# Kernel tuning notes

Measured on AMD Instinct MI355X. Metric: run time of the kernel, lower is better.

The kernel has to match this reference:

```python
import jax, jax.numpy as jnp
import numpy as np

B, C, KF, VF, H, W = 16, 128, 128, 128, 128, 128


def setup_inputs() -> dict:
    key = jax.random.key(0)
    k1, k2, k3, k4, k5 = jax.random.split(key, 5)
    x = jax.random.normal(k1, (B, C, H, W), dtype=jnp.float32)
    # 1x1 conv weights (flattened to [out_ch, in_ch]); small init so raw exp stays finite
    qk_w = jax.random.normal(k2, (2 * KF, 2 * C), dtype=jnp.float32) * 0.02
    qk_b = jnp.zeros((2 * KF,), dtype=jnp.float32)
    v_w = jax.random.normal(k3, (VF, C), dtype=jnp.float32) * 0.02
    v_b = jnp.zeros((VF,), dtype=jnp.float32)
    return {"x": x, "qk_w": qk_w, "qk_b": qk_b, "v_w": v_w, "v_b": v_b}


def reference(x, qk_w, qk_b, v_w, v_b):
    Bc, Cc, Hc, Wc = x.shape
    # qk 1x1 conv on channel-doubled input: (B, 2*KF, H, W)
    x_qk = jnp.concatenate([x, x], axis=1)
    qk = jnp.einsum('oc,bchw->bohw', qk_w, x_qk) + qk_b[None, :, None, None]
    q, k = jnp.split(qk, 2, axis=1)  # each (B, KF, H, W)
    # scores over row positions: contract the W axis -> (B, KF, H, H)
    scores = jnp.einsum('bfhw,bfgw->bfhg', q, k) * (Cc ** -0.5)
    # hand-rolled causal softmax: raw exp * lower-triangular mask / sum (no max subtraction, faithful)
    mask = jnp.tril(jnp.ones((Hc, Hc), dtype=scores.dtype))  # mask[r, c] = 1 iff r >= c
    masked_exps = jnp.exp(scores) * mask[None, None, :, :]
    causal_softmax = masked_exps / masked_exps.sum(axis=-1, keepdims=True)
    # v 1x1 conv: (B, VF, H, W)
    v = jnp.einsum('oc,bchw->bohw', v_w, x) + v_b[None, :, None, None]
    # einsum 'jilm,jklm->jklm' == v * sum over the KF axis of the softmax
    out = v * causal_softmax.sum(axis=1, keepdims=True)
    return out
```

## Files before the change

kernel.cpp:

```cpp
#include <hip/hip_runtime.h>
#include <hip/hip_bf16.h>


using short8 = __attribute__((ext_vector_type(8))) short;
using f32x4  = __attribute__((ext_vector_type(4))) float;
typedef unsigned short u16;
typedef unsigned int   u32;
typedef unsigned char  u8;

#define NB 16
#define NC 128
#define NP 16384
#define TILES_QK 4
#define TILES_V 8
#define NFG 16
#define SCALE 0.08838834764831845f

__device__ inline u16 f2bf(float f) {
  u32 u = __float_as_uint(f);
  return (u16)((u + 0x7FFFu + ((u >> 16) & 1u)) >> 16);
}
__device__ inline u32 pk2(float a, float b) {
  union { __hip_bfloat162 h; u32 u; } cv;
  cv.h = __float22bfloat162_rn(make_float2(a, b));
  return cv.u;
}
__device__ inline f32x4 fz4(){ f32x4 z; z[0]=0.f; z[1]=0.f; z[2]=0.f; z[3]=0.f; return z; }
__device__ inline long u2l(uint2 v){ union{uint2 u; long l;} c; c.u = v; return c.l; }
__device__ inline int kap(int r){ return ((r ^ (r >> 2)) & 15) << 4; }

__device__ inline void barrier_lgkm() {
  __builtin_amdgcn_sched_barrier(0);
  asm volatile("s_waitcnt lgkmcnt(0)" ::: "memory");
  __builtin_amdgcn_s_barrier();
  __builtin_amdgcn_sched_barrier(0);
}

__global__ __launch_bounds__(256) void prep_w(
    const float* __restrict__ qk_w, const float* __restrict__ v_w,
    u16* __restrict__ Weff, u16* __restrict__ Vw) {
  const int i = blockIdx.x * 256 + threadIdx.x;
  #pragma unroll
  for (int r = 0; r < 2; ++r) {
    const int e = i * 2 + r;
    const int f = e >> 7, c = e & 127;
    Weff[e] = f2bf(qk_w[f * 256 + c] + qk_w[f * 256 + 128 + c]);
  }
  Vw[i] = f2bf(v_w[i]);
}

__device__ inline void stage_issue(const float* __restrict__ xb, int tid,
                                   float4& r0, float4& r1, float4& r2, float4& r3) {
  const int c0 = (tid >> 4) * 4, p0 = (tid & 15) * 4;
  r0 = *(const float4*)(xb + (size_t)(c0 + 0) * NP + p0);
  r1 = *(const float4*)(xb + (size_t)(c0 + 1) * NP + p0);
  r2 = *(const float4*)(xb + (size_t)(c0 + 2) * NP + p0);
  r3 = *(const float4*)(xb + (size_t)(c0 + 3) * NP + p0);
}
__device__ inline void stage_write(u16* xs, int tid,
                                   float4 r0, float4 r1, float4 r2, float4 r3) {
  const int c0 = (tid >> 4) * 4, p0 = (tid & 15) * 4;
  const float* a0 = (const float*)&r0;
  const float* a1 = (const float*)&r1;
  const float* a2 = (const float*)&r2;
  const float* a3 = (const float*)&r3;
  #pragma unroll
  for (int j = 0; j < 4; ++j) {
    const int p = p0 + j;
    uint2 pk;
    pk.x = pk2(a0[j], a1[j]);
    pk.y = pk2(a2[j], a3[j]);
    *(uint2*)((char*)xs + p * 256 + ((c0 * 2) ^ kap(p))) = pk;
  }
}

__global__ __launch_bounds__(512, 2) void qk_conv(
    const float* __restrict__ x, const u16* __restrict__ Weff,
    const float* __restrict__ qk_b, u8* __restrict__ QK) {
  __shared__ u16 xs[2][64 * 128];
  __shared__ char rb[8][2048];
  const int b = blockIdx.y, tg = blockIdx.x, tid = threadIdx.x;
  const int wv = tid >> 6, l = tid & 63, l15 = l & 15, lq = l >> 4;
  const float* xb = x + (size_t)b * NC * NP + tg * (64 * TILES_QK);

  short8 wf[4][2];
  #pragma unroll
  for (int ks = 0; ks < 4; ++ks) {
    const int cc = ks * 32 + lq * 8;
    wf[ks][0] = *(const short8*)(Weff + (size_t)(wv * 32 + l15) * 128 + cc);
    wf[ks][1] = *(const short8*)(Weff + (size_t)(wv * 32 + 16 + l15) * 128 + cc);
  }
  const float bias0 = qk_b[wv * 32 + l15];
  const float bias1 = qk_b[wv * 32 + 16 + l15];

  float4 r0, r1, r2, r3;
  stage_issue(xb, tid, r0, r1, r2, r3);
  stage_write(xs[0], tid, r0, r1, r2, r3);

  for (int t = 0; t < TILES_QK; ++t) {
    if (t + 1 < TILES_QK) stage_issue(xb + (t + 1) * 64, tid, r0, r1, r2, r3);
    barrier_lgkm();

    const u16* cur = xs[t & 1];
    f32x4 acc[4][2];
    #pragma unroll
    for (int m = 0; m < 4; ++m) { acc[m][0] = fz4(); acc[m][1] = fz4(); }
    #pragma unroll
    for (int ks = 0; ks < 4; ++ks) {
      const int cc2 = (ks * 32 + lq * 8) * 2;
      #pragma unroll
      for (int m = 0; m < 4; ++m) {
        const int p = m * 16 + l15;
        short8 af = *(const short8*)((const char*)cur + p * 256 + (cc2 ^ kap(p)));
        acc[m][0] = __builtin_amdgcn_mfma_f32_16x16x32_bf16(af, wf[ks][0], acc[m][0], 0, 0, 0);
        acc[m][1] = __builtin_amdgcn_mfma_f32_16x16x32_bf16(af, wf[ks][1], acc[m][1], 0, 0, 0);
      }
    }

    if (t + 1 < TILES_QK) stage_write(xs[(t + 1) & 1], tid, r0, r1, r2, r3);

    const int pbase = tg * (64 * TILES_QK) + t * 64;
    char* rbw = rb[wv];
    #pragma unroll
    for (int n = 0; n < 2; ++n) {
      const int fl = n * 16 + l15;
      const float bias = n ? bias1 : bias0;
      #pragma unroll
      for (int m = 0; m < 4; ++m) {
        int pk4 = __builtin_amdgcn_cvt_pk_fp8_f32(acc[m][n][0] + bias,
                                                  acc[m][n][1] + bias, 0, false);
        pk4 = __builtin_amdgcn_cvt_pk_fp8_f32(acc[m][n][2] + bias,
                                              acc[m][n][3] + bias, pk4, true);
        *(int*)(rbw + fl * 64 + ((m ^ (fl & 3)) * 16) + lq * 4) = pk4;
      }
    }
    #pragma unroll
    for (int i = 0; i < 2; ++i) {
      const int r = i * 16 + (l >> 2);
      const int pg = l & 3, lg = pg ^ (r & 3);
      uint4 v = *(const uint4*)(rbw + r * 64 + pg * 16);
      *(uint4*)((char*)QK + (((size_t)(b * 256 + wv * 32 + r)) << 14)
                + pbase + lg * 16) = v;
    }
  }
}

__global__ __launch_bounds__(512, 2) void scores_softmax(
    const u8* __restrict__ QK, float* __restrict__ Spart) {
  __shared__ u8 Ksm[2][16384];
  const int b = blockIdx.y, fg = blockIdx.x, tid = threadIdx.x;
  const int wv = tid >> 6, l = tid & 63, l15 = l & 15, lq = l >> 4;
  const int hbase = wv * 16;

  int srcoff[2];
  #pragma unroll
  for (int s = 0; s < 2; ++s) {
    const int a = s * 512 + tid;
    const int g = a >> 3, gr = a & 7;
    srcoff[s] = ((a & ~7) | (gr ^ ((g >> 1) & 7))) * 16;
  }

  {
    const char* kp = (const char*)QK + (((size_t)(b * 256 + 128 + fg * 8)) << 14);
    #pragma unroll
    for (int s = 0; s < 2; ++s)
      *(uint4*)((char*)Ksm[0] + (s * 512 + tid) * 16) = *(const uint4*)(kp + srcoff[s]);
  }
  __syncthreads();

  float Sacc[8][4];
  #pragma unroll
  for (int n = 0; n < 8; ++n)
    #pragma unroll
    for (int r = 0; r < 4; ++r) Sacc[n][r] = 0.f;

  for (int fi = 0; fi < 8; ++fi) {
    const u8* kb = Ksm[fi & 1];
    const bool pf = (fi < 7);
    uint4 st0, st1;
    if (pf) {
      const char* kp = (const char*)QK + (((size_t)(b * 256 + 128 + fg * 8 + fi + 1)) << 14);
      st0 = *(const uint4*)(kp + srcoff[0]);
      st1 = *(const uint4*)(kp + srcoff[1]);
    }

    const char* Qp = (const char*)QK + (((size_t)(b * 256 + fg * 8 + fi)) << 14);
    f32x4 acc[8];
    #pragma unroll
    for (int n = 0; n < 8; ++n) acc[n] = fz4();
    #pragma unroll
    for (int ks = 0; ks < 4; ++ks) {
      const int hq = hbase + l15;
      uint2 aq = *(const uint2*)(Qp + hq * 128 + ks * 32 + lq * 8);
      const long a8 = u2l(aq);
      #pragma unroll
      for (int n = 0; n < 8; ++n) {
        const int g = n * 16 + l15;
        uint2 bq = *(const uint2*)((const char*)kb + g * 128
                                   + (((ks * 4 + lq) ^ (g & 14)) << 3));
        acc[n] = __builtin_amdgcn_mfma_f32_16x16x32_fp8_fp8(a8, u2l(bq), acc[n], 0, 0, 0);
      }
    }

    float part[4] = {0.f, 0.f, 0.f, 0.f};
    #pragma unroll
    for (int n = 0; n < 8; ++n)
      #pragma unroll
      for (int r = 0; r < 4; ++r) {
        const int h = hbase + lq * 4 + r;
        const int g = n * 16 + l15;
        float e = (g <= h) ? __expf(acc[n][r] * SCALE) : 0.f;
        acc[n][r] = e;
        part[r] += e;
      }
    #pragma unroll
    for (int r = 0; r < 4; ++r) {
      part[r] += __shfl_xor(part[r], 1);
      part[r] += __shfl_xor(part[r], 2);
      part[r] += __shfl_xor(part[r], 4);
      part[r] += __shfl_xor(part[r], 8);
    }
    #pragma unroll
    for (int r = 0; r < 4; ++r) part[r] = 1.0f / part[r];
    #pragma unroll
    for (int n = 0; n < 8; ++n)
      #pragma unroll
      for (int r = 0; r < 4; ++r) Sacc[n][r] += acc[n][r] * part[r];

    if (pf) {
      char* kd = (char*)Ksm[(fi & 1) ^ 1];
      *(uint4*)(kd + (0 * 512 + tid) * 16) = st0;
      *(uint4*)(kd + (1 * 512 + tid) * 16) = st1;
    }
    __syncthreads();
  }

  float* Sp = Spart + ((size_t)(fg * NB + b)) * NP;
  #pragma unroll
  for (int n = 0; n < 8; ++n)
    #pragma unroll
    for (int r = 0; r < 4; ++r) {
      const int h = hbase + lq * 4 + r, g = n * 16 + l15;
      Sp[h * 128 + g] = Sacc[n][r];
    }
}

__device__ inline void v_compute(const u16* cur, int l15, int lq,
                                 f32x4 acc[4], const short8 wf[4]) {
  #pragma unroll
  for (int m = 0; m < 4; ++m) acc[m] = fz4();
  #pragma unroll
  for (int ks = 0; ks < 4; ++ks) {
    const int cc2 = (ks * 32 + lq * 8) * 2;
    #pragma unroll
    for (int m = 0; m < 4; ++m) {
      const int p = m * 16 + l15;
      short8 af = *(const short8*)((const char*)cur + p * 256 + (cc2 ^ kap(p)));
      acc[m] = __builtin_amdgcn_mfma_f32_16x16x32_bf16(af, wf[ks], acc[m], 0, 0, 0);
    }
  }
}
__device__ inline void v_store(float* orow, const float* Ssm, int lq,
                               const f32x4 acc[4], int pbase, int ploc, float vb) {
  #pragma unroll
  for (int m = 0; m < 4; ++m) {
    const int o = m * 16 + lq * 4;
    float4 sv = *(const float4*)(Ssm + ploc + o);
    float4 oo;
    oo.x = (acc[m][0] + vb) * sv.x;
    oo.y = (acc[m][1] + vb) * sv.y;
    oo.z = (acc[m][2] + vb) * sv.z;
    oo.w = (acc[m][3] + vb) * sv.w;
    *(float4*)(orow + pbase + o) = oo;
  }
}

__global__ __launch_bounds__(512, 2) void v_conv_mul(
    const float* __restrict__ x, const u16* __restrict__ Vw,
    const float* __restrict__ v_b, const float* __restrict__ Spart,
    float* __restrict__ out) {
  __shared__ u16 xs[2][64 * 128];
  __shared__ float Ssm[512];
  const int b = blockIdx.y, tg = blockIdx.x, tid = threadIdx.x;
  const int wv = tid >> 6, l = tid & 63, l15 = l & 15, lq = l >> 4;
  const float* xb = x + (size_t)b * NC * NP + tg * (64 * TILES_V);

  short8 wf[4];
  #pragma unroll
  for (int ks = 0; ks < 4; ++ks)
    wf[ks] = *(const short8*)(Vw + (size_t)(wv * 16 + l15) * 128 + ks * 32 + lq * 8);
  const int f = wv * 16 + l15;
  const float vb = v_b[f];
  float* orow = out + (size_t)(b * 128 + f) * NP;

  {
    const size_t poff = (size_t)b * NP + tg * 512 + tid;
    float s = 0.f;
    #pragma unroll
    for (int q = 0; q < NFG; ++q) s += Spart[(size_t)q * NB * NP + poff];
    Ssm[tid] = s;
  }

  float4 A0, A1, A2, A3, B0, B1, B2, B3;
  stage_issue(xb, tid, A0, A1, A2, A3);
  stage_write(xs[0], tid, A0, A1, A2, A3);
  stage_issue(xb + 64, tid, B0, B1, B2, B3);

  f32x4 acc[4];
  #pragma unroll
  for (int tp = 0; tp < TILES_V; tp += 2) {
    barrier_lgkm();
    if (tp + 2 < TILES_V) stage_issue(xb + (tp + 2) * 64, tid, A0, A1, A2, A3);
    v_compute(xs[0], l15, lq, acc, wf);
    if (tp + 1 < TILES_V) stage_write(xs[1], tid, B0, B1, B2, B3);
    v_store(orow, Ssm, lq, acc, tg * (64 * TILES_V) + tp * 64, tp * 64, vb);
    barrier_lgkm();
    if (tp + 3 < TILES_V) stage_issue(xb + (tp + 3) * 64, tid, B0, B1, B2, B3);
    v_compute(xs[1], l15, lq, acc, wf);
    if (tp + 2 < TILES_V) stage_write(xs[0], tid, A0, A1, A2, A3);
    v_store(orow, Ssm, lq, acc, tg * (64 * TILES_V) + (tp + 1) * 64, (tp + 1) * 64, vb);
  }
}

extern "C" void kernel_launch(void* const* d_in, const int* in_sizes, int n_in,
                              void* d_out, int out_size, void* d_ws, size_t ws_size,
                              hipStream_t stream) {
  const float* x    = (const float*)d_in[0];
  const float* qk_w = (const float*)d_in[1];
  const float* qk_b = (const float*)d_in[2];
  const float* v_w  = (const float*)d_in[3];
  const float* v_b  = (const float*)d_in[4];
  float* out = (float*)d_out;

  char* ws = (char*)d_ws;
  u8*    QK    = (u8*)ws;
  float* Spart = (float*)(ws + (size_t)67108864);
  u16*   Weff  = (u16*)(ws + (size_t)67108864 + 16777216);
  u16*   Vw    = (u16*)(ws + (size_t)67108864 + 16777216 + 65536);

  prep_w<<<64, 256, 0, stream>>>(qk_w, v_w, Weff, Vw);
  qk_conv<<<dim3(64, 16), 512, 0, stream>>>(x, Weff, qk_b, QK);
  scores_softmax<<<dim3(16, 16), 512, 0, stream>>>(QK, Spart);
  v_conv_mul<<<dim3(32, 16), 512, 0, stream>>>(x, Vw, v_b, Spart, out);
}
```

Measured before the change: 127.0 us.

## Split qk_conv output features across two blocks with 256 threads each

The qk 1x1 conv kernel now launches a third grid dimension that splits the 256 output features into two halves, each handled by a 256-thread block of four waves. Every thread stages eight input float4 loads instead of four, so a smaller block still loads the full 64x128 input tile. This doubles the number of blocks and shrinks each block, which aims to improve occupancy and scheduling. In exchange, each input tile is read from global memory and converted to bf16 twice, once per feature half.

```diff
diff --git a/kernel.cpp b/kernel.cpp
--- a/kernel.cpp
+++ b/kernel.cpp
@@ -74,31 +74,72 @@
   }
 }
 
-__global__ __launch_bounds__(512, 2) void qk_conv(
+__device__ inline void stage_issue256(const float* __restrict__ xb, int tid,
+                                      float4& s0, float4& s1, float4& s2, float4& s3,
+                                      float4& s4, float4& s5, float4& s6, float4& s7) {
+  const int c0 = (tid >> 4) * 4, p0 = (tid & 15) * 4;
+  s0 = *(const float4*)(xb + (size_t)(c0 + 0) * NP + p0);
+  s1 = *(const float4*)(xb + (size_t)(c0 + 1) * NP + p0);
+  s2 = *(const float4*)(xb + (size_t)(c0 + 2) * NP + p0);
+  s3 = *(const float4*)(xb + (size_t)(c0 + 3) * NP + p0);
+  s4 = *(const float4*)(xb + (size_t)(c0 + 64) * NP + p0);
+  s5 = *(const float4*)(xb + (size_t)(c0 + 65) * NP + p0);
+  s6 = *(const float4*)(xb + (size_t)(c0 + 66) * NP + p0);
+  s7 = *(const float4*)(xb + (size_t)(c0 + 67) * NP + p0);
+}
+__device__ inline void stage_write256(u16* xs, int tid,
+                                      float4 s0, float4 s1, float4 s2, float4 s3,
+                                      float4 s4, float4 s5, float4 s6, float4 s7) {
+  const int c0 = (tid >> 4) * 4, p0 = (tid & 15) * 4;
+  const float* a0 = (const float*)&s0;
+  const float* a1 = (const float*)&s1;
+  const float* a2 = (const float*)&s2;
+  const float* a3 = (const float*)&s3;
+  const float* a4 = (const float*)&s4;
+  const float* a5 = (const float*)&s5;
+  const float* a6 = (const float*)&s6;
+  const float* a7 = (const float*)&s7;
+  #pragma unroll
+  for (int j = 0; j < 4; ++j) {
+    const int p = p0 + j;
+    uint2 pk0, pk1;
+    pk0.x = pk2(a0[j], a1[j]);
+    pk0.y = pk2(a2[j], a3[j]);
+    pk1.x = pk2(a4[j], a5[j]);
+    pk1.y = pk2(a6[j], a7[j]);
+    char* row = (char*)xs + p * 256;
+    *(uint2*)(row + ((c0 * 2) ^ kap(p))) = pk0;
+    *(uint2*)(row + (((c0 + 64) * 2) ^ kap(p))) = pk1;
+  }
+}
+
+__global__ __launch_bounds__(256, 2) void qk_conv(
     const float* __restrict__ x, const u16* __restrict__ Weff,
     const float* __restrict__ qk_b, u8* __restrict__ QK) {
   __shared__ u16 xs[2][64 * 128];
-  __shared__ char rb[8][2048];
-  const int b = blockIdx.y, tg = blockIdx.x, tid = threadIdx.x;
+  __shared__ char rb[4][2048];
+  const int b = blockIdx.y, tg = blockIdx.x, half = blockIdx.z, tid = threadIdx.x;
   const int wv = tid >> 6, l = tid & 63, l15 = l & 15, lq = l >> 4;
+  const int fw = half * 128 + wv * 32;
   const float* xb = x + (size_t)b * NC * NP + tg * (64 * TILES_QK);
 
   short8 wf[4][2];
   #pragma unroll
   for (int ks = 0; ks < 4; ++ks) {
     const int cc = ks * 32 + lq * 8;
-    wf[ks][0] = *(const short8*)(Weff + (size_t)(wv * 32 + l15) * 128 + cc);
-    wf[ks][1] = *(const short8*)(Weff + (size_t)(wv * 32 + 16 + l15) * 128 + cc);
-  }
-  const float bias0 = qk_b[wv * 32 + l15];
-  const float bias1 = qk_b[wv * 32 + 16 + l15];
-
-  float4 r0, r1, r2, r3;
-  stage_issue(xb, tid, r0, r1, r2, r3);
-  stage_write(xs[0], tid, r0, r1, r2, r3);
+    wf[ks][0] = *(const short8*)(Weff + (size_t)(fw + l15) * 128 + cc);
+    wf[ks][1] = *(const short8*)(Weff + (size_t)(fw + 16 + l15) * 128 + cc);
+  }
+  const float bias0 = qk_b[fw + l15];
+  const float bias1 = qk_b[fw + 16 + l15];
+
+  float4 s0, s1, s2, s3, s4, s5, s6, s7;
+  stage_issue256(xb, tid, s0, s1, s2, s3, s4, s5, s6, s7);
+  stage_write256(xs[0], tid, s0, s1, s2, s3, s4, s5, s6, s7);
 
   for (int t = 0; t < TILES_QK; ++t) {
-    if (t + 1 < TILES_QK) stage_issue(xb + (t + 1) * 64, tid, r0, r1, r2, r3);
+    if (t + 1 < TILES_QK)
+      stage_issue256(xb + (t + 1) * 64, tid, s0, s1, s2, s3, s4, s5, s6, s7);
     barrier_lgkm();
 
     const u16* cur = xs[t & 1];
@@ -117,7 +158,8 @@
       }
     }
 
-    if (t + 1 < TILES_QK) stage_write(xs[(t + 1) & 1], tid, r0, r1, r2, r3);
+    if (t + 1 < TILES_QK)
+      stage_write256(xs[(t + 1) & 1], tid, s0, s1, s2, s3, s4, s5, s6, s7);
 
     const int pbase = tg * (64 * TILES_QK) + t * 64;
     char* rbw = rb[wv];
@@ -139,7 +181,7 @@
       const int r = i * 16 + (l >> 2);
       const int pg = l & 3, lg = pg ^ (r & 3);
       uint4 v = *(const uint4*)(rbw + r * 64 + pg * 16);
-      *(uint4*)((char*)QK + (((size_t)(b * 256 + wv * 32 + r)) << 14)
+      *(uint4*)((char*)QK + (((size_t)(b * 256 + fw + r)) << 14)
                 + pbase + lg * 16) = v;
     }
   }
@@ -339,7 +381,7 @@
   u16*   Vw    = (u16*)(ws + (size_t)67108864 + 16777216 + 65536);
 
   prep_w<<<64, 256, 0, stream>>>(qk_w, v_w, Weff, Vw);
-  qk_conv<<<dim3(64, 16), 512, 0, stream>>>(x, Weff, qk_b, QK);
+  qk_conv<<<dim3(64, 16, 2), 256, 0, stream>>>(x, Weff, qk_b, QK);
   scores_softmax<<<dim3(16, 16), 512, 0, stream>>>(QK, Spart);
   v_conv_mul<<<dim3(32, 16), 512, 0, stream>>>(x, Vw, v_b, Spart, out);
 }
```

Result: slower. 137.1 us (+8.0%).
